# Optimization experiments

Hardware: AMD Instinct MI355X
Metric: run time of the kernel (lower is better)

## Reference

```python
import jax, jax.numpy as jnp
import numpy as np

B, L, H, HKV, D, E = 2, 2048, 8, 1, 256, 2048
SCALING = D ** -0.5


def rotate_half(x):
    x1, x2 = jnp.split(x, 2, axis=-1)
    return jnp.concatenate([-x2, x1], axis=-1)


def setup_inputs() -> dict:
    key = jax.random.key(0)
    ks = jax.random.split(key, 5)
    hidden_states = jax.random.normal(ks[0], (B, L, E), jnp.float32)
    attention_mask = jnp.zeros((B, 1, 1, L, L), jnp.float32)  # additive mask (all visible)
    # standard RoPE tables, shape [L, D]
    inv_freq = 1.0 / (10000.0 ** (jnp.arange(0, D, 2, dtype=jnp.float32) / D))
    freqs = jnp.arange(L, dtype=jnp.float32)[:, None] * inv_freq[None, :]
    emb = jnp.concatenate([freqs, freqs], axis=-1)
    cos, sin = jnp.cos(emb), jnp.sin(emb)
    s = 0.02
    Wq = jax.random.normal(ks[1], (H * D, E), jnp.float32) * s
    Wk = jax.random.normal(ks[2], (HKV * D, E), jnp.float32) * s
    Wv = jax.random.normal(ks[3], (HKV * D, E), jnp.float32) * s
    Wo = jax.random.normal(ks[4], (E, H * D), jnp.float32) * s
    return {"hidden_states": hidden_states, "attention_mask": attention_mask,
            "cos": cos, "sin": sin, "Wq": Wq, "Wk": Wk, "Wv": Wv, "Wo": Wo}


def reference(hidden_states, attention_mask, cos, sin, Wq, Wk, Wv, Wo):
    b, l, _ = hidden_states.shape
    q = jnp.einsum('ble,de->bld', hidden_states, Wq)
    k = jnp.einsum('ble,de->bld', hidden_states, Wk)
    v = jnp.einsum('ble,de->bld', hidden_states, Wv)
    # q: [B, L, 1, H, D] -> transpose(1,3) -> [B, H, 1, L, D]
    q = jnp.transpose(q.reshape(b, l, 1, H, D), (0, 3, 2, 1, 4))
    # k, v: [B, 1, L, Hkv, D] -> transpose(2,3) -> [B, 1, Hkv, L, D]
    k = jnp.transpose(k.reshape(b, 1, l, HKV, D), (0, 1, 3, 2, 4))
    v = jnp.transpose(v.reshape(b, 1, l, HKV, D), (0, 1, 3, 2, 4))
    # RoPE (cos/sin broadcast over leading dims)
    q = q * cos + rotate_half(q) * sin
    k = k * cos + rotate_half(k) * sin
    # scores: [B, H, Hkv, L, L]
    attn = jnp.matmul(q, jnp.swapaxes(k, -1, -2)) * SCALING
    attn = attn + attention_mask
    attn = jax.nn.softmax(attn.astype(jnp.float32), axis=-1)
    out = jnp.matmul(attn, v)                         # [B, H, Hkv, L, D]
    out = jnp.transpose(out, (0, 1, 3, 2, 4))         # [B, H, L, Hkv, D]
    out = out.reshape(b, l, H * D)                    # row-major reshape, as torch .reshape
    return jnp.einsum('bld,ed->ble', out, Wo)
```

## Files before the change

kernel.cpp:

```cpp
#include <hip/hip_runtime.h>

typedef unsigned short u16;
typedef __attribute__((ext_vector_type(8))) short short8;
typedef __attribute__((ext_vector_type(4))) float f32x4;
typedef __attribute__((ext_vector_type(16))) float f32x16;

struct __align__(8) US4 { u16 x, y, z, w; };

__device__ __forceinline__ u16 f2bf(float x) {
  union { float f; unsigned u; } c; c.f = x;
  unsigned r = c.u + 0x7fffu + ((c.u >> 16) & 1u);
  return (u16)(r >> 16);
}
__device__ __forceinline__ float bf2f(u16 u) {
  union { unsigned u; float f; } c; c.u = ((unsigned)u) << 16;
  return c.f;
}
__device__ __forceinline__ void gload_lds16(const void* g, void* l) {
  __builtin_amdgcn_global_load_lds(
      (const __attribute__((address_space(1))) void*)g,
      (__attribute__((address_space(3))) void*)l, 16, 0, 0);
}
__device__ __forceinline__ f32x4 fzero4() {
  f32x4 z; z[0] = 0.f; z[1] = 0.f; z[2] = 0.f; z[3] = 0.f; return z;
}

__global__ __launch_bounds__(256) void cvt_all(
    const float* __restrict__ h, const float* __restrict__ wq,
    const float* __restrict__ wk, const float* __restrict__ wv,
    const float* __restrict__ wo, u16* __restrict__ Xbf,
    u16* __restrict__ Wqkv, u16* __restrict__ Wob) {
  int b = blockIdx.x;
  const float* s; u16* d; int off;
  if (b < 8192)       { s = h;  d = Xbf;            off = b; }
  else if (b < 12288) { s = wq; d = Wqkv;           off = b - 8192; }
  else if (b < 12800) { s = wk; d = Wqkv + 4194304; off = b - 12288; }
  else if (b < 13312) { s = wv; d = Wqkv + 4718592; off = b - 12800; }
  else                { s = wo; d = Wob;            off = b - 13312; }
  int i = (off * 256 + threadIdx.x) * 4;
  float4 v = *(const float4*)(s + i);
  US4 o = { f2bf(v.x), f2bf(v.y), f2bf(v.z), f2bf(v.w) };
  *(US4*)(d + i) = o;
}

template <int MODE>
__global__ __launch_bounds__(256) void gemm_nt(
    const u16* __restrict__ A, const u16* __restrict__ Bw,
    u16* __restrict__ q_out, u16* __restrict__ k_out, u16* __restrict__ v_out,
    float* __restrict__ c_out) {
  __shared__ u16 lA[128 * 32];
  __shared__ u16 lB[128 * 32];
  const int K = 2048;
  int t = threadIdx.x, w = t >> 6, lane = t & 63;
  int wm = w >> 1, wn = w & 1;
  int m0 = blockIdx.x * 128, n0 = blockIdx.y * 128;
  int g = lane >> 4, qi = lane & 15;

  f32x4 acc[4][4];
#pragma unroll
  for (int i = 0; i < 4; i++)
#pragma unroll
    for (int j = 0; j < 4; j++) acc[i][j] = fzero4();

  for (int k0 = 0; k0 < K; k0 += 32) {
#pragma unroll
    for (int i = 0; i < 2; i++) {
      int off = i * 4096 + w * 1024 + lane * 16;
      int row = off >> 6, cg = (off >> 4) & 3;
      gload_lds16(A + (size_t)(m0 + row) * K + k0 + cg * 8,
                  (char*)lA + i * 4096 + w * 1024);
      gload_lds16(Bw + (size_t)(n0 + row) * K + k0 + cg * 8,
                  (char*)lB + i * 4096 + w * 1024);
    }
    __syncthreads();
    short8 af[4], bfr[4];
#pragma unroll
    for (int f = 0; f < 4; f++) {
      int ra = wm * 64 + f * 16 + qi;
      int rb = wn * 64 + f * 16 + qi;
      int kb2 = g * 16;
      af[f] = *(const short8*)((const char*)lA + ra * 64 + kb2);
      bfr[f] = *(const short8*)((const char*)lB + rb * 64 + kb2);
    }
#pragma unroll
    for (int i = 0; i < 4; i++)
#pragma unroll
      for (int j = 0; j < 4; j++)
        acc[i][j] = __builtin_amdgcn_mfma_f32_16x16x32_bf16(af[i], bfr[j], acc[i][j], 0, 0, 0);
    __syncthreads();
  }

#pragma unroll
  for (int i = 0; i < 4; i++) {
#pragma unroll
    for (int j = 0; j < 4; j++) {
#pragma unroll
      for (int r = 0; r < 4; r++) {
        int m = m0 + wm * 64 + i * 16 + g * 4 + r;
        int n = n0 + wn * 64 + j * 16 + qi;
        float v = acc[i][j][r];
        if (MODE == 0) {
          int b = m >> 11, l = m & 2047;
          if (n < 2048) {
            int hh = n >> 8, dd = n & 255;
            q_out[(((size_t)(b * 8 + hh) * 2048) + l) * 256 + dd] = f2bf(v);
          } else if (n < 2304) {
            int dd = n - 2048;
            k_out[((size_t)b * 2048 + l) * 256 + dd] = f2bf(v);
          } else {
            int dd = n - 2304;
            v_out[((size_t)b * 256 + dd) * 2048 + l] = f2bf(v);
          }
        } else {
          c_out[(size_t)m * 2048 + n] = v;
        }
      }
    }
  }
}

__global__ __launch_bounds__(256) void rope_kernel(u16* __restrict__ q, u16* __restrict__ k,
                                                   const float* __restrict__ cosT,
                                                   const float* __restrict__ sinT) {
  int idx = blockIdx.x * 2 + (threadIdx.x >> 7);
  int d = threadIdx.x & 127;
  u16* ptr;
  int l;
  float sc;
  if (idx < 32768) { ptr = q + (size_t)idx * 256; l = idx & 2047; sc = 0.0625f; }
  else             { ptr = k + (size_t)(idx - 32768) * 256; l = (idx - 32768) & 2047; sc = 1.0f; }
  float x1 = bf2f(ptr[d]), x2 = bf2f(ptr[d + 128]);
  float c1 = cosT[l * 256 + d], s1 = sinT[l * 256 + d];
  float c2 = cosT[l * 256 + d + 128], s2 = sinT[l * 256 + d + 128];
  float o1 = (x1 * c1 - x2 * s1) * sc;
  float o2 = (x2 * c2 + x1 * s2) * sc;
  ptr[d] = f2bf(o1);
  ptr[d + 128] = f2bf(o2);
}

__global__ __launch_bounds__(512, 2) void flash_kernel(
    const u16* __restrict__ qr, const u16* __restrict__ kr,
    const u16* __restrict__ vt_g, u16* __restrict__ attnout) {
  __shared__ __align__(16) char lds[147456];

  int t = threadIdx.x, w = t >> 6, lane = t & 63;
  int lo5 = lane & 31, hi = lane >> 5;
  int half = w >> 2, wl = w & 3;
  int b = blockIdx.z, h = blockIdx.y;
  int bh = b * 8 + h;
  int l0 = blockIdx.x * 128;
  int qrow = l0 + wl * 32 + lo5;

  const u16* kb = kr + (size_t)b * (2048 * 256);
  const u16* vb = vt_g + (size_t)b * (256 * 2048);
  char* unitbase = lds + half * 65536;
  char* plw = lds + 131072 + w * 2048;
  int kvbase = half * 1024;

  short8 qf[16];
  {
    const u16* qb = qr + ((size_t)bh * 2048 + qrow) * 256 + hi * 8;
#pragma unroll
    for (int ks = 0; ks < 16; ks++) qf[ks] = *(const short8*)(qb + ks * 16);
  }

  f32x16 ot[8];
#pragma unroll
  for (int dv = 0; dv < 8; dv++)
#pragma unroll
    for (int r = 0; r < 16; r++) ot[dv][r] = 0.f;
  float mrow = -1e30f, lrow = 0.f;

  auto stage = [&](int buf, int it) {
    char* unit = unitbase + buf * 32768;
    int kvg = kvbase + it * 32;
#pragma unroll
    for (int i = 0; i < 4; i++) {
      int dbase = i * 4096 + wl * 1024;
      int off = dbase + lane * 16;
      {
        int row = off >> 9, slot = (off >> 4) & 31;
        int ss = slot ^ (row & 7);
        gload_lds16(kb + (size_t)(kvg + row) * 256 + ss * 8, unit + dbase);
      }
      {
        int dd = off >> 6, slot = (off >> 4) & 3;
        int ss = slot ^ ((dd >> 1) & 3);
        gload_lds16(vb + (size_t)dd * 2048 + kvg + ss * 8, unit + 16384 + dbase);
      }
    }
  };

  stage(0, 0);
  __syncthreads();

  for (int it = 0; it < 32; ++it) {
    int buf = it & 1;
    if (it < 31) stage(buf ^ 1, it + 1);
    char* unit = unitbase + buf * 32768;

    f32x16 st;
#pragma unroll
    for (int r = 0; r < 16; r++) st[r] = 0.f;
#pragma unroll
    for (int ks = 0; ks < 16; ks++) {
      int ss = (2 * ks + hi) ^ (lo5 & 7);
      short8 kf = *(const short8*)(unit + lo5 * 512 + ss * 16);
      st = __builtin_amdgcn_mfma_f32_32x32x16_bf16(kf, qf[ks], st, 0, 0, 0);
    }

    float tmax = st[0];
#pragma unroll
    for (int r = 1; r < 16; r++) tmax = fmaxf(tmax, st[r]);
    tmax = fmaxf(tmax, __shfl_xor(tmax, 32));
    if (__any(tmax > mrow)) {
      float mnew = fmaxf(mrow, tmax);
      float scale = __expf(mrow - mnew);
#pragma unroll
      for (int dv = 0; dv < 8; dv++)
#pragma unroll
        for (int r = 0; r < 16; r++) ot[dv][r] *= scale;
      lrow *= scale;
      mrow = mnew;
    }
    float tsum = 0.f;
#pragma unroll
    for (int r = 0; r < 16; r++) {
      float p = __expf(st[r] - mrow);
      st[r] = p;
      tsum += p;
    }
    tsum += __shfl_xor(tsum, 32);
    lrow += tsum;

#pragma unroll
    for (int r4 = 0; r4 < 4; r4++) {
      US4 pw = { f2bf(st[4 * r4 + 0]), f2bf(st[4 * r4 + 1]),
                 f2bf(st[4 * r4 + 2]), f2bf(st[4 * r4 + 3]) };
      int byte_ = lo5 * 64 + ((r4 ^ ((lo5 >> 1) & 3)) << 4) + hi * 8;
      *(US4*)(plw + byte_) = pw;
    }

#pragma unroll
    for (int jks = 0; jks < 2; jks++) {
      int ps = ((2 * jks + hi) ^ ((lo5 >> 1) & 3)) << 4;
      short8 pf = *(const short8*)(plw + lo5 * 64 + ps);
#pragma unroll
      for (int dv = 0; dv < 8; dv++) {
        int dd = dv * 32 + lo5;
        int ss = (2 * jks + hi) ^ ((dd >> 1) & 3);
        short8 vf = *(const short8*)(unit + 16384 + dd * 64 + ss * 16);
        ot[dv] = __builtin_amdgcn_mfma_f32_32x32x16_bf16(vf, pf, ot[dv], 0, 0, 0);
      }
    }
    __syncthreads();
  }

  char* chunk = lds + wl * 32768;
  float* mlx = (float*)(lds + 131072 + wl * 4096);
  if (half == 0) {
#pragma unroll
    for (int dv = 0; dv < 8; dv++)
#pragma unroll
      for (int r4 = 0; r4 < 4; r4++) {
        f32x4 v;
        v[0] = ot[dv][4 * r4 + 0]; v[1] = ot[dv][4 * r4 + 1];
        v[2] = ot[dv][4 * r4 + 2]; v[3] = ot[dv][4 * r4 + 3];
        *(f32x4*)(chunk + ((dv * 4 + r4) * 64 + lane) * 16) = v;
      }
    mlx[lane * 2 + 0] = mrow;
    mlx[lane * 2 + 1] = lrow;
  }
  __syncthreads();
  if (half == 1) {
    float mA = mlx[lane * 2 + 0], lA = mlx[lane * 2 + 1];
    float m = fmaxf(mA, mrow);
    float cA = __expf(mA - m), cB = __expf(mrow - m);
    float linv = 1.f / (lA * cA + lrow * cB);
    u16* ob = attnout + ((size_t)bh * 2048 + qrow) * 256;
#pragma unroll
    for (int dv = 0; dv < 8; dv++)
#pragma unroll
      for (int r4 = 0; r4 < 4; r4++) {
        f32x4 oA = *(const f32x4*)(chunk + ((dv * 4 + r4) * 64 + lane) * 16);
        US4 o;
        o.x = f2bf((oA[0] * cA + ot[dv][4 * r4 + 0] * cB) * linv);
        o.y = f2bf((oA[1] * cA + ot[dv][4 * r4 + 1] * cB) * linv);
        o.z = f2bf((oA[2] * cA + ot[dv][4 * r4 + 2] * cB) * linv);
        o.w = f2bf((oA[3] * cA + ot[dv][4 * r4 + 3] * cB) * linv);
        *(US4*)(ob + dv * 32 + 8 * r4 + 4 * hi) = o;
      }
  }
}

extern "C" void kernel_launch(void* const* d_in, const int* in_sizes, int n_in,
                              void* d_out, int out_size, void* d_ws, size_t ws_size,
                              hipStream_t stream) {
  const float* hidden = (const float*)d_in[0];
  const float* cosT = (const float*)d_in[2];
  const float* sinT = (const float*)d_in[3];
  const float* Wq = (const float*)d_in[4];
  const float* Wk = (const float*)d_in[5];
  const float* Wv = (const float*)d_in[6];
  const float* Wo = (const float*)d_in[7];

  char* ws = (char*)d_ws;
  u16* Xbf  = (u16*)(ws + 0);
  u16* Wqkv = (u16*)(ws + 16777216);
  u16* Wob  = (u16*)(ws + 27262976);
  u16* qbuf = (u16*)(ws + 35651584);
  u16* kbuf = (u16*)(ws + 52428800);
  u16* vT   = (u16*)(ws + 54525952);
  u16* attn = (u16*)(ws + 56623104);
  float* out = (float*)d_out;

  cvt_all<<<17408, 256, 0, stream>>>(hidden, Wq, Wk, Wv, Wo, Xbf, Wqkv, Wob);
  gemm_nt<0><<<dim3(32, 20), 256, 0, stream>>>(Xbf, Wqkv, qbuf, kbuf, vT, nullptr);
  rope_kernel<<<18432, 256, 0, stream>>>(qbuf, kbuf, cosT, sinT);
  flash_kernel<<<dim3(16, 8, 2), 512, 0, stream>>>(qbuf, kbuf, vT, attn);
  gemm_nt<1><<<dim3(32, 16), 256, 0, stream>>>(attn, Wob, nullptr, nullptr, nullptr, out);
}
```

Baseline: 281.0 us.

## Remap GEMM tiles, repack P in registers via permlane swap, raise MFMA priority

The GEMM kernel remaps workgroup IDs so consecutive blocks are interleaved in groups of eight, which is meant to improve L2 locality across chiplets. In the flash kernel the P tile is converted to bf16 with packed v_cvt_pk_bf16_f32 and rearranged with v_permlane32_swap instead of a round trip through LDS. s_setprio is raised around the MFMA loops to favour matrix issue. The register repack depends on the permlane swap matching the MFMA operand layout, and the tile remap assumes the tile count divides by eight.

```diff
diff --git a/kernel.cpp b/kernel.cpp
--- a/kernel.cpp
+++ b/kernel.cpp
@@ -23,6 +23,11 @@
 }
 __device__ __forceinline__ f32x4 fzero4() {
   f32x4 z; z[0] = 0.f; z[1] = 0.f; z[2] = 0.f; z[3] = 0.f; return z;
+}
+__device__ __forceinline__ unsigned cvtpk(float lo, float hi) {
+  unsigned r;
+  asm("v_cvt_pk_bf16_f32 %0, %1, %2" : "=v"(r) : "v"(lo), "v"(hi));
+  return r;
 }
 
 __global__ __launch_bounds__(256) void cvt_all(
@@ -53,7 +58,13 @@
   const int K = 2048;
   int t = threadIdx.x, w = t >> 6, lane = t & 63;
   int wm = w >> 1, wn = w & 1;
-  int m0 = blockIdx.x * 128, n0 = blockIdx.y * 128;
+
+  int gx = gridDim.x;
+  int wg = blockIdx.y * gx + blockIdx.x;
+  int per = (gx * gridDim.y) >> 3;
+  int nid = (wg & 7) * per + (wg >> 3);
+  int m0 = (nid % gx) * 128, n0 = (nid / gx) * 128;
+
   int g = lane >> 4, qi = lane & 15;
 
   f32x4 acc[4][4];
@@ -154,7 +165,6 @@
   const u16* kb = kr + (size_t)b * (2048 * 256);
   const u16* vb = vt_g + (size_t)b * (256 * 2048);
   char* unitbase = lds + half * 65536;
-  char* plw = lds + 131072 + w * 2048;
   int kvbase = half * 1024;
 
   short8 qf[16];
@@ -179,13 +189,11 @@
       int dbase = i * 4096 + wl * 1024;
       int off = dbase + lane * 16;
       {
-        int row = off >> 9, slot = (off >> 4) & 31;
-        int ss = slot ^ (row & 7);
+        int row = off >> 9, slot = (off >> 4) & 31, ss = slot ^ (row & 7);
         gload_lds16(kb + (size_t)(kvg + row) * 256 + ss * 8, unit + dbase);
       }
       {
-        int dd = off >> 6, slot = (off >> 4) & 3;
-        int ss = slot ^ ((dd >> 1) & 3);
+        int dd = off >> 6, slot = (off >> 4) & 3, ss = slot ^ ((dd >> 1) & 3);
         gload_lds16(vb + (size_t)dd * 2048 + kvg + ss * 8, unit + 16384 + dbase);
       }
     }
@@ -202,12 +210,14 @@
     f32x16 st;
 #pragma unroll
     for (int r = 0; r < 16; r++) st[r] = 0.f;
+    __builtin_amdgcn_s_setprio(1);
 #pragma unroll
     for (int ks = 0; ks < 16; ks++) {
       int ss = (2 * ks + hi) ^ (lo5 & 7);
       short8 kf = *(const short8*)(unit + lo5 * 512 + ss * 16);
       st = __builtin_amdgcn_mfma_f32_32x32x16_bf16(kf, qf[ks], st, 0, 0, 0);
     }
+    __builtin_amdgcn_s_setprio(0);
 
     float tmax = st[0];
 #pragma unroll
@@ -234,17 +244,19 @@
     lrow += tsum;
 
 #pragma unroll
-    for (int r4 = 0; r4 < 4; r4++) {
-      US4 pw = { f2bf(st[4 * r4 + 0]), f2bf(st[4 * r4 + 1]),
-                 f2bf(st[4 * r4 + 2]), f2bf(st[4 * r4 + 3]) };
-      int byte_ = lo5 * 64 + ((r4 ^ ((lo5 >> 1) & 3)) << 4) + hi * 8;
-      *(US4*)(plw + byte_) = pw;
-    }
-
-#pragma unroll
     for (int jks = 0; jks < 2; jks++) {
-      int ps = ((2 * jks + hi) ^ ((lo5 >> 1) & 3)) << 4;
-      short8 pf = *(const short8*)(plw + lo5 * 64 + ps);
+      union { unsigned u[4]; short8 s; } pfu;
+      {
+        unsigned a0 = cvtpk(st[8 * jks + 0], st[8 * jks + 1]);
+        unsigned a1 = cvtpk(st[8 * jks + 2], st[8 * jks + 3]);
+        unsigned b0 = cvtpk(st[8 * jks + 4], st[8 * jks + 5]);
+        unsigned b1 = cvtpk(st[8 * jks + 6], st[8 * jks + 7]);
+        asm("v_permlane32_swap_b32 %0, %1" : "+v"(a0), "+v"(b0));
+        asm("v_permlane32_swap_b32 %0, %1" : "+v"(a1), "+v"(b1));
+        pfu.u[0] = a0; pfu.u[1] = a1; pfu.u[2] = b0; pfu.u[3] = b1;
+      }
+      short8 pf = pfu.s;
+      __builtin_amdgcn_s_setprio(1);
 #pragma unroll
       for (int dv = 0; dv < 8; dv++) {
         int dd = dv * 32 + lo5;
@@ -252,6 +264,7 @@
         short8 vf = *(const short8*)(unit + 16384 + dd * 64 + ss * 16);
         ot[dv] = __builtin_amdgcn_mfma_f32_32x32x16_bf16(vf, pf, ot[dv], 0, 0, 0);
       }
+      __builtin_amdgcn_s_setprio(0);
     }
     __syncthreads();
   }
```

Measured after the change: 273.5 us. 1.03x faster.
